# Kernel optimization log

Hardware: AMD Instinct MI355X
Metric: run time of the kernel (lower is better)

The kernel has to match this reference:

```python
import jax, jax.numpy as jnp
import numpy as np

T_STEPS = 128
N_RAYS = 16384
RAY_EXT = 10.0  # ray_ext_factor


def _posenc(x, n_freq=4):
    # x: (...,3) in [-1,1] -> (...,3 + 3*2*n_freq) = (...,27)
    feats = [x]
    for k in range(n_freq):
        f = (2.0 ** k) * jnp.pi
        feats.append(jnp.sin(f * x))
        feats.append(jnp.cos(f * x))
    return jnp.concatenate(feats, -1)


def _sh_deg2(d):
    # real spherical harmonics, degree 0 and 1 (4 coeffs), d unit vectors (...,3)
    x, y, z = d[..., 0], d[..., 1], d[..., 2]
    c0 = 0.28209479177387814
    c1 = 0.4886025119029199
    return jnp.stack([jnp.full_like(x, c0), c1 * y, c1 * z, c1 * x], -1)


def _forward(rays_o, rays_d, tnoise, aabb, W1, b1, W2, b2, Wc1, bc1, Wc2, bc2):
    # --- ray-AABB intersection (slab method), RayBundle.intersect_aabb ---
    inv_d = 1.0 / rays_d
    t0 = (aabb[0] - rays_o) * inv_d
    t1 = (aabb[1] - rays_o) * inv_d
    tnear = jnp.maximum(jnp.max(jnp.minimum(t0, t1), -1, keepdims=True), 0.0)  # (N,1)
    tfar = jnp.min(jnp.maximum(t0, t1), -1, keepdims=True)                      # (N,1)
    active = (tfar > tnear).astype(rays_o.dtype)  # active_mask; masking replaces compaction

    # --- StratifiedRayStepSampler: ts (T,N,1) ---
    T = tnoise.shape[0]
    base = (jnp.arange(T, dtype=rays_o.dtype)[:, None, None] + tnoise) / T
    ts = tnear[None] + (tfar - tnear)[None] * base
    xyz = rays_o[None] + ts * rays_d[None]  # (T,N,3)

    # --- vol.sample(xyz, ynm, return_color=True): density + color MLP ---
    xn = 2.0 * (xyz - aabb[0]) / (aabb[1] - aabb[0]) - 1.0
    enc = _posenc(xn)                             # (T,N,27)
    h = jax.nn.relu(enc @ W1 + b1)                # (T,N,64)
    dh = h @ W2 + b2                              # (T,N,16)
    sigma = jnp.exp(dh[..., :1])                  # (T,N,1) density
    feat = dh[..., 1:]                            # (T,N,15)
    dnorm = jnp.linalg.norm(rays_d, axis=-1, keepdims=True)  # (N,1)
    ynm = _sh_deg2(rays_d / dnorm)                # encode_raydir -> (N,4)
    ynm = jnp.broadcast_to(ynm[None], (T,) + ynm.shape)      # expand to (T,N,4)
    hc = jax.nn.relu(jnp.concatenate([feat, ynm], -1) @ Wc1 + bc1)
    rgb = jax.nn.sigmoid(hc @ Wc2 + bc2)          # (T,N,3)

    # --- integrate_timesteps: transmittance-weighted compositing ---
    tfinal = tfar * RAY_EXT
    delta = jnp.concatenate([ts[1:] - ts[:-1], tfinal[None] - ts[-1:]], 0)  # (T,N,1)
    sd = sigma * delta * dnorm[None]
    alpha = 1.0 - jnp.exp(-sd)
    trans = jnp.exp(-(jnp.cumsum(sd, 0) - sd))    # exclusive cumsum transmittance
    w = trans * alpha * active[None]              # (T,N,1); inactive rays -> zero maps

    color = jnp.sum(w * rgb, 0)                   # color_map  (N,3)
    alpha_map = jnp.sum(w, 0)                     # alpha_map  (N,1)
    return jnp.concatenate([color, alpha_map], -1)  # rgba (N,4)


def setup_inputs() -> dict:
    key = jax.random.key(0)
    ks = jax.random.split(key, 8)
    # origins on a sphere of radius 2.5 around the unit aabb, aimed at points inside it
    o = jax.random.normal(ks[0], (N_RAYS, 3), jnp.float32)
    o = 2.5 * o / jnp.linalg.norm(o, axis=-1, keepdims=True)
    tgt = jax.random.uniform(ks[1], (N_RAYS, 3), jnp.float32, -0.5, 0.5)
    d = tgt - o
    d = d / jnp.linalg.norm(d, axis=-1, keepdims=True)
    aabb = jnp.array([[-1.0, -1.0, -1.0], [1.0, 1.0, 1.0]], jnp.float32)
    tnoise = jax.random.uniform(ks[2], (T_STEPS, N_RAYS, 1), jnp.float32)
    s1, s2, s3, s4 = 27 ** -0.5, 64 ** -0.5, 19 ** -0.5, 64 ** -0.5
    return {
        'rays_o': o, 'rays_d': d, 'tnoise': tnoise, 'aabb': aabb,
        'W1': jax.random.normal(ks[3], (27, 64), jnp.float32) * s1,
        'b1': jnp.zeros((64,), jnp.float32),
        'W2': jax.random.normal(ks[4], (64, 16), jnp.float32) * (0.1 * s2),
        'b2': jnp.zeros((16,), jnp.float32),
        'Wc1': jax.random.normal(ks[5], (19, 64), jnp.float32) * s3,
        'bc1': jnp.zeros((64,), jnp.float32),
        'Wc2': jax.random.normal(ks[6], (64, 3), jnp.float32) * s4,
        'bc2': jnp.zeros((3,), jnp.float32),
    }


def reference(rays_o, rays_d, tnoise, aabb, W1, b1, W2, b2, Wc1, bc1, Wc2, bc2):
    return _forward(rays_o, rays_d, tnoise, aabb, W1, b1, W2, b2, Wc1, bc1, Wc2, bc2)
```

## Files before the change

### kernel.cpp

```cpp
#include <hip/hip_runtime.h>
#include <stdint.h>

#define N_RAYS  16384
#define T_STEPS 128
#define RPW   16
#define WAVES 4
#define TSEG  16

typedef _Float16 half8  __attribute__((ext_vector_type(8)));
typedef _Float16 half4  __attribute__((ext_vector_type(4)));
typedef __fp16   fp16x2 __attribute__((ext_vector_type(2)));
typedef float    float4_ __attribute__((ext_vector_type(4)));

#define H_W2K   2048
#define H_WC1K  3072
#define H_WC2K  4096
#define F32_CV  2560
#define F32_BC2 2880
#define F32_S0  2896
#define F32_PART 4096

__device__ __forceinline__ uint32_t pk(float a, float b) {
    fp16x2 h = __builtin_amdgcn_cvt_pkrtz(a, b);
    return __builtin_bit_cast(uint32_t, h);
}
__device__ __forceinline__ uint32_t pkr(float a, float b) {
    fp16x2 h = __builtin_amdgcn_cvt_pkrtz(a, b);
    fp16x2 z = {(__fp16)0.f, (__fp16)0.f};
    fp16x2 m = __builtin_elementwise_max(h, z);
    return __builtin_bit_cast(uint32_t, m);
}
__device__ __forceinline__ half4 mk4(uint32_t lo, uint32_t hi) {
    union { uint32_t u[2]; half4 h; } v;
    v.u[0] = lo; v.u[1] = hi;
    return v.h;
}

__global__ void prep_weights(const float* __restrict__ W1, const float* __restrict__ b1,
                             const float* __restrict__ W2, const float* __restrict__ b2,
                             const float* __restrict__ Wc1, const float* __restrict__ bc1,
                             const float* __restrict__ Wc2, const float* __restrict__ bc2,
                             void* __restrict__ ws) {
    _Float16* wh = (_Float16*)ws;
    float*    wf = (float*)ws;
    int frag = blockIdx.x;
    int lane = threadIdx.x;
    int mm = lane & 15, q = lane >> 4;
    if (frag < 4) {
        int tau = frag;
        int n = tau * 16 + mm;
        for (int j = 0; j < 8; ++j) {
            float w;
            if (j < 6)      w = W1[(3 + 6 * q + j) * 64 + n];
            else if (j == 6) w = (q == 0) ? W1[0 * 64 + n] : (q == 1) ? W1[2 * 64 + n] : 0.f;
            else             w = (q == 0) ? W1[1 * 64 + n] : (q == 1) ? b1[n] : 0.f;
            wh[(tau * 64 + lane) * 8 + j] = (_Float16)w;
        }
    } else if (frag < 8) {
        int tau = frag - 4;
        for (int j = 0; j < 4; ++j) {
            int k = 16 * tau + 4 * q + j;
            wh[H_W2K + (tau * 64 + lane) * 4 + j] = (_Float16)W2[k * 16 + mm];
        }
    } else if (frag < 12) {
        int tau = frag - 8;
        int n2 = tau * 16 + mm;
        for (int j = 0; j < 4; ++j) {
            int k = 4 * q + j;
            float w = (k == 0) ? 0.f : Wc1[(k - 1) * 64 + n2];
            wh[H_WC1K + (tau * 64 + lane) * 4 + j] = (_Float16)w;
        }
    } else if (frag < 16) {
        int tau = frag - 12;
        for (int j = 0; j < 4; ++j) {
            int k = 16 * tau + 4 * q + j;
            wh[H_WC2K + (tau * 64 + lane) * 4 + j] =
                (_Float16)((mm < 3) ? Wc2[k * 3 + mm] : 0.f);
        }
    } else {
        int n = lane;
        wf[F32_CV + 0 * 64 + n] = Wc1[15 * 64 + n];
        wf[F32_CV + 1 * 64 + n] = Wc1[16 * 64 + n];
        wf[F32_CV + 2 * 64 + n] = Wc1[17 * 64 + n];
        wf[F32_CV + 3 * 64 + n] = Wc1[18 * 64 + n];
        float cc = bc1[n];
        for (int c = 0; c < 15; ++c) cc += b2[1 + c] * Wc1[c * 64 + n];
        wf[F32_CV + 4 * 64 + n] = cc;
        if (lane < 16) wf[F32_BC2 + lane] = (lane < 3) ? bc2[lane] : 0.f;
        if (lane == 0) wf[F32_S0] = b2[0];
    }
}

__global__ __launch_bounds__(256, 4)
void render_kernel(const float* __restrict__ rays_o, const float* __restrict__ rays_d,
                   const float* __restrict__ tnoise, const float* __restrict__ aabb,
                   void* __restrict__ ws, float* __restrict__ out) {
    __shared__ float sComb[WAVES][RPW][5];

    const int tid  = threadIdx.x;
    const int wv   = tid >> 6;
    const int lane = tid & 63;
    const int m    = lane & 15;
    const int q    = lane >> 4;
    const int half_ = blockIdx.x & 1;
    const int rb   = blockIdx.x >> 1;
    const int r    = rb * RPW + m;

    const half8* wsv   = (const half8*)ws;
    const half4* w2k   = (const half4*)((const _Float16*)ws + H_W2K);
    const half4* wc1k  = (const half4*)((const _Float16*)ws + H_WC1K);
    const half4* wc2k  = (const half4*)((const _Float16*)ws + H_WC2K);
    const float* wsf   = (const float*)ws;
    half8 fW1[4];
    half4 fW2[4], fWc1[4], fWc2[4];
    #pragma unroll
    for (int i = 0; i < 4; ++i) fW1[i]  = wsv[i * 64 + lane];
    #pragma unroll
    for (int i = 0; i < 4; ++i) fW2[i]  = w2k[i * 64 + lane];
    #pragma unroll
    for (int i = 0; i < 4; ++i) fWc1[i] = wc1k[i * 64 + lane];
    #pragma unroll
    for (int i = 0; i < 4; ++i) fWc2[i] = wc2k[i * 64 + lane];
    const float4_ binit = ((const float4_*)(wsf + F32_BC2))[q];
    const float s0b = wsf[F32_S0];

    float o0 = rays_o[r * 3 + 0], o1 = rays_o[r * 3 + 1], o2 = rays_o[r * 3 + 2];
    float d0 = rays_d[r * 3 + 0], d1 = rays_d[r * 3 + 1], d2 = rays_d[r * 3 + 2];
    float a00 = aabb[0], a01 = aabb[1], a02 = aabb[2];
    float a10 = aabb[3], a11 = aabb[4], a12 = aabb[5];

    float i0 = 1.0f / d0, i1 = 1.0f / d1, i2 = 1.0f / d2;
    float u0 = (a00 - o0) * i0, v0 = (a10 - o0) * i0;
    float u1 = (a01 - o1) * i1, v1 = (a11 - o1) * i1;
    float u2 = (a02 - o2) * i2, v2 = (a02 * 0.0f + a12 - o2) * i2;
    float tnear = fmaxf(fmaxf(fmaxf(fminf(u0, v0), fminf(u1, v1)), fminf(u2, v2)), 0.0f);
    float tfar  = fminf(fminf(fmaxf(u0, v0), fmaxf(u1, v1)), fmaxf(u2, v2));
    bool active = (tfar > tnear);
    float dt = tfar - tnear;
    float dt128 = dt * (1.0f / 128.0f);

    float dn  = sqrtf(d0 * d0 + d1 * d1 + d2 * d2);
    float idn = 1.0f / dn;
    const float c0sh = 0.28209479177387814f;
    const float c1sh = 0.4886025119029199f;
    float y1 = c1sh * d1 * idn, y2 = c1sh * d2 * idn, y3 = c1sh * d0 * idn;

    float4_ cv[4];
    #pragma unroll
    for (int tau = 0; tau < 4; ++tau) {
        #pragma unroll
        for (int reg = 0; reg < 4; ++reg) {
            int n = tau * 16 + 4 * q + reg;
            float c = wsf[F32_CV + 4 * 64 + n];
            c = fmaf(c0sh, wsf[F32_CV + 0 * 64 + n], c);
            c = fmaf(y1,   wsf[F32_CV + 1 * 64 + n], c);
            c = fmaf(y2,   wsf[F32_CV + 2 * 64 + n], c);
            c = fmaf(y3,   wsf[F32_CV + 3 * 64 + n], c);
            cv[tau][reg] = c;
        }
    }

    float qs = 0.5f * (float)(1 << q);
    float sc0 = 2.0f / (a10 - a00), of0 = -a00 * sc0 - 1.0f;
    float sc1 = 2.0f / (a11 - a01), of1 = -a01 * sc1 - 1.0f;
    float sc2 = 2.0f / (a12 - a02), of2 = -a02 * sc2 - 1.0f;
    float scq0 = sc0 * qs, ofq0 = of0 * qs;
    float scq1 = sc1 * qs, ofq1 = of1 * qs;
    float scq2 = sc2 * qs, ofq2 = of2 * qs;

    const float4_ z4 = {0.f, 0.f, 0.f, 0.f};
    const bool q0 = (q == 0), q1 = (q == 1);

    float trans = 1.0f, sdtot = 0.0f, wacc = 0.0f;
    float cacc0 = 0.0f, cacc1 = 0.0f, cacc2 = 0.0f;

    const int tbase = half_ * 64 + wv * TSEG;
    float nA = tnoise[(tbase + 0) * N_RAYS + r];
    float nB = tnoise[(tbase + 1) * N_RAYS + r];

    #pragma unroll 1
    for (int tt = 0; tt < TSEG; tt += 2) {
        const int t0 = tbase + tt, t1 = t0 + 1;
        float nC = (t0 + 2 < T_STEPS) ? tnoise[(t0 + 2) * N_RAYS + r] : 0.0f;
        float nD = (t0 + 3 < T_STEPS) ? tnoise[(t0 + 3) * N_RAYS + r] : 0.0f;
        float ts0 = fmaf((float)t0 + nA, dt128, tnear);
        float ts1 = fmaf((float)t1 + nB, dt128, tnear);
        float ts2 = fmaf((float)(t0 + 2) + nC, dt128, tnear);
        float tsP[2] = {ts0, ts1};
        float deltaP[2];
        deltaP[0] = ts1 - ts0;
        deltaP[1] = (t1 < T_STEPS - 1) ? (ts2 - ts1) : fmaf(tfar, 10.0f, -ts1);
        nA = nC; nB = nD;

        float dhx[2];
        float4_ rgbP[2];

        #pragma unroll
        for (int p = 0; p < 2; ++p) {
            float x = fmaf(tsP[p], d0, o0);
            float y = fmaf(tsP[p], d1, o1);
            float z = fmaf(tsP[p], d2, o2);
            float xr0 = fmaf(x, scq0, ofq0);
            float xr1 = fmaf(y, scq1, ofq1);
            float xr2 = fmaf(z, scq2, ofq2);
            float s0 = __builtin_amdgcn_sinf(xr0);
            float s1 = __builtin_amdgcn_sinf(xr1);
            float s2 = __builtin_amdgcn_sinf(xr2);
            float cA = __builtin_amdgcn_cosf(xr0);
            float cB = __builtin_amdgcn_cosf(xr1);
            float cC = __builtin_amdgcn_cosf(xr2);
            float e6 = q0 ? (xr0 + xr0) : (q1 ? xr2 : 0.0f);
            float e7 = q0 ? (xr1 + xr1) : (q1 ? 1.0f : 0.0f);
            union { uint32_t u[4]; half8 h; } xf_;
            xf_.u[0] = pk(s0, s1); xf_.u[1] = pk(s2, cA);
            xf_.u[2] = pk(cB, cC); xf_.u[3] = pk(e6, e7);
            half8 xf = xf_.h;

            float4_ h0 = __builtin_amdgcn_mfma_f32_16x16x32_f16(fW1[0], xf, z4, 0, 0, 0);
            float4_ h1 = __builtin_amdgcn_mfma_f32_16x16x32_f16(fW1[1], xf, z4, 0, 0, 0);
            float4_ h2 = __builtin_amdgcn_mfma_f32_16x16x32_f16(fW1[2], xf, z4, 0, 0, 0);
            float4_ h3 = __builtin_amdgcn_mfma_f32_16x16x32_f16(fW1[3], xf, z4, 0, 0, 0);

            half4 hB0 = mk4(pkr(h0.x, h0.y), pkr(h0.z, h0.w));
            half4 hB1 = mk4(pkr(h1.x, h1.y), pkr(h1.z, h1.w));
            half4 hB2 = mk4(pkr(h2.x, h2.y), pkr(h2.z, h2.w));
            half4 hB3 = mk4(pkr(h3.x, h3.y), pkr(h3.z, h3.w));

            float4_ dh = __builtin_amdgcn_mfma_f32_16x16x16f16(fW2[0], hB0, z4, 0, 0, 0);
            dh = __builtin_amdgcn_mfma_f32_16x16x16f16(fW2[1], hB1, dh, 0, 0, 0);
            dh = __builtin_amdgcn_mfma_f32_16x16x16f16(fW2[2], hB2, dh, 0, 0, 0);
            dh = __builtin_amdgcn_mfma_f32_16x16x16f16(fW2[3], hB3, dh, 0, 0, 0);
            dhx[p] = dh.x;

            half4 fb = mk4(pk(dh.x, dh.y), pk(dh.z, dh.w));

            float4_ t0v = __builtin_amdgcn_mfma_f32_16x16x16f16(fWc1[0], fb, cv[0], 0, 0, 0);
            float4_ t1v = __builtin_amdgcn_mfma_f32_16x16x16f16(fWc1[1], fb, cv[1], 0, 0, 0);
            float4_ t2v = __builtin_amdgcn_mfma_f32_16x16x16f16(fWc1[2], fb, cv[2], 0, 0, 0);
            float4_ t3v = __builtin_amdgcn_mfma_f32_16x16x16f16(fWc1[3], fb, cv[3], 0, 0, 0);

            half4 cB0 = mk4(pkr(t0v.x, t0v.y), pkr(t0v.z, t0v.w));
            half4 cB1 = mk4(pkr(t1v.x, t1v.y), pkr(t1v.z, t1v.w));
            half4 cB2 = mk4(pkr(t2v.x, t2v.y), pkr(t2v.z, t2v.w));
            half4 cB3 = mk4(pkr(t3v.x, t3v.y), pkr(t3v.z, t3v.w));

            float4_ rgb = __builtin_amdgcn_mfma_f32_16x16x16f16(fWc2[0], cB0, binit, 0, 0, 0);
            rgb = __builtin_amdgcn_mfma_f32_16x16x16f16(fWc2[1], cB1, rgb, 0, 0, 0);
            rgb = __builtin_amdgcn_mfma_f32_16x16x16f16(fWc2[2], cB2, rgb, 0, 0, 0);
            rgb = __builtin_amdgcn_mfma_f32_16x16x16f16(fWc2[3], cB3, rgb, 0, 0, 0);
            rgbP[p] = rgb;
        }

        if (q == 0) {
            #pragma unroll
            for (int p = 0; p < 2; ++p) {
                float sigma = __expf(dhx[p] + s0b);
                float sd = sigma * deltaP[p] * dn;
                float e = __expf(-sd);
                float alpha = 1.0f - e;
                float w = trans * alpha;
                float rr = __builtin_amdgcn_rcpf(1.0f + __expf(-rgbP[p].x));
                float rg = __builtin_amdgcn_rcpf(1.0f + __expf(-rgbP[p].y));
                float rb = __builtin_amdgcn_rcpf(1.0f + __expf(-rgbP[p].z));
                cacc0 = fmaf(w, rr, cacc0);
                cacc1 = fmaf(w, rg, cacc1);
                cacc2 = fmaf(w, rb, cacc2);
                wacc += w;
                trans *= e;
                sdtot += sd;
            }
        }
    }

    if (q == 0) {
        sComb[wv][m][0] = sdtot;
        sComb[wv][m][1] = wacc;
        sComb[wv][m][2] = cacc0;
        sComb[wv][m][3] = cacc1;
        sComb[wv][m][4] = cacc2;
    }
    __syncthreads();

    if (tid < RPW) {
        float P = 1.0f, C0 = 0.0f, C1 = 0.0f, C2 = 0.0f, WS = 0.0f, SD = 0.0f;
        #pragma unroll
        for (int s = 0; s < WAVES; ++s) {
            C0 = fmaf(P, sComb[s][tid][2], C0);
            C1 = fmaf(P, sComb[s][tid][3], C1);
            C2 = fmaf(P, sComb[s][tid][4], C2);
            WS = fmaf(P, sComb[s][tid][1], WS);
            SD += sComb[s][tid][0];
            P *= __expf(-sComb[s][tid][0]);
        }
        const int rg = rb * RPW + tid;
        float* part = (float*)ws + F32_PART + (half_ * N_RAYS + rg) * 6;
        part[0] = SD;
        part[1] = WS;
        part[2] = C0;
        part[3] = C1;
        part[4] = C2;
        part[5] = active ? 1.0f : 0.0f;
    }
}

__global__ __launch_bounds__(256)
void combine_kernel(const void* __restrict__ ws, float* __restrict__ out) {
    int r = blockIdx.x * 256 + threadIdx.x;
    const float* pa = (const float*)ws + F32_PART + r * 6;
    const float* pb = (const float*)ws + F32_PART + (N_RAYS + r) * 6;
    float P = __expf(-pa[0]);
    float act = pa[5];
    out[r * 4 + 0] = fmaf(P, pb[2], pa[2]) * act;
    out[r * 4 + 1] = fmaf(P, pb[3], pa[3]) * act;
    out[r * 4 + 2] = fmaf(P, pb[4], pa[4]) * act;
    out[r * 4 + 3] = fmaf(P, pb[1], pa[1]) * act;
}

extern "C" void kernel_launch(void* const* d_in, const int* in_sizes, int n_in,
                              void* d_out, int out_size, void* d_ws, size_t ws_size,
                              hipStream_t stream) {
    const float* rays_o = (const float*)d_in[0];
    const float* rays_d = (const float*)d_in[1];
    const float* tnoise = (const float*)d_in[2];
    const float* aabb   = (const float*)d_in[3];
    const float* W1  = (const float*)d_in[4];
    const float* b1  = (const float*)d_in[5];
    const float* W2  = (const float*)d_in[6];
    const float* b2  = (const float*)d_in[7];
    const float* Wc1 = (const float*)d_in[8];
    const float* bc1 = (const float*)d_in[9];
    const float* Wc2 = (const float*)d_in[10];
    const float* bc2 = (const float*)d_in[11];

    prep_weights<<<dim3(17), dim3(64), 0, stream>>>(W1, b1, W2, b2, Wc1, bc1, Wc2, bc2, d_ws);

    dim3 grid(2 * N_RAYS / RPW);
    dim3 block(WAVES * 64);
    render_kernel<<<grid, block, 0, stream>>>(rays_o, rays_d, tnoise, aabb, d_ws,
                                              (float*)d_out);

    combine_kernel<<<dim3(N_RAYS / 256), dim3(256), 0, stream>>>(d_ws, (float*)d_out);
}
```

Baseline: 124.8 us.

## Drop weight-prep kernel, load weights inline and split MFMA accumulation chains

Removes the separate prep_weights launch. Each render wave now gathers and converts the MLP weights to fp16 fragments directly from the raw inputs, and folds the b2/Wc1 constant vector in place. This removes one kernel launch and its serialization before the render kernel. In exchange, every block does many more scattered scalar global loads and conversions at startup, and the bias-fold fma loop is recomputed per thread. Separately, the 4-deep dependent MFMA chains for the second and output layers are split into two independent chains that are summed, to shorten the dependency latency.

```diff
diff --git a/kernel.cpp b/kernel.cpp
--- a/kernel.cpp
+++ b/kernel.cpp
@@ -12,13 +12,7 @@
 typedef __fp16   fp16x2 __attribute__((ext_vector_type(2)));
 typedef float    float4_ __attribute__((ext_vector_type(4)));
 
-#define H_W2K   2048
-#define H_WC1K  3072
-#define H_WC2K  4096
-#define F32_CV  2560
-#define F32_BC2 2880
-#define F32_S0  2896
-#define F32_PART 4096
+#define F32_PART 0
 
 __device__ __forceinline__ uint32_t pk(float a, float b) {
     fp16x2 h = __builtin_amdgcn_cvt_pkrtz(a, b);
@@ -36,65 +30,14 @@
     return v.h;
 }
 
-__global__ void prep_weights(const float* __restrict__ W1, const float* __restrict__ b1,
-                             const float* __restrict__ W2, const float* __restrict__ b2,
-                             const float* __restrict__ Wc1, const float* __restrict__ bc1,
-                             const float* __restrict__ Wc2, const float* __restrict__ bc2,
-                             void* __restrict__ ws) {
-    _Float16* wh = (_Float16*)ws;
-    float*    wf = (float*)ws;
-    int frag = blockIdx.x;
-    int lane = threadIdx.x;
-    int mm = lane & 15, q = lane >> 4;
-    if (frag < 4) {
-        int tau = frag;
-        int n = tau * 16 + mm;
-        for (int j = 0; j < 8; ++j) {
-            float w;
-            if (j < 6)      w = W1[(3 + 6 * q + j) * 64 + n];
-            else if (j == 6) w = (q == 0) ? W1[0 * 64 + n] : (q == 1) ? W1[2 * 64 + n] : 0.f;
-            else             w = (q == 0) ? W1[1 * 64 + n] : (q == 1) ? b1[n] : 0.f;
-            wh[(tau * 64 + lane) * 8 + j] = (_Float16)w;
-        }
-    } else if (frag < 8) {
-        int tau = frag - 4;
-        for (int j = 0; j < 4; ++j) {
-            int k = 16 * tau + 4 * q + j;
-            wh[H_W2K + (tau * 64 + lane) * 4 + j] = (_Float16)W2[k * 16 + mm];
-        }
-    } else if (frag < 12) {
-        int tau = frag - 8;
-        int n2 = tau * 16 + mm;
-        for (int j = 0; j < 4; ++j) {
-            int k = 4 * q + j;
-            float w = (k == 0) ? 0.f : Wc1[(k - 1) * 64 + n2];
-            wh[H_WC1K + (tau * 64 + lane) * 4 + j] = (_Float16)w;
-        }
-    } else if (frag < 16) {
-        int tau = frag - 12;
-        for (int j = 0; j < 4; ++j) {
-            int k = 16 * tau + 4 * q + j;
-            wh[H_WC2K + (tau * 64 + lane) * 4 + j] =
-                (_Float16)((mm < 3) ? Wc2[k * 3 + mm] : 0.f);
-        }
-    } else {
-        int n = lane;
-        wf[F32_CV + 0 * 64 + n] = Wc1[15 * 64 + n];
-        wf[F32_CV + 1 * 64 + n] = Wc1[16 * 64 + n];
-        wf[F32_CV + 2 * 64 + n] = Wc1[17 * 64 + n];
-        wf[F32_CV + 3 * 64 + n] = Wc1[18 * 64 + n];
-        float cc = bc1[n];
-        for (int c = 0; c < 15; ++c) cc += b2[1 + c] * Wc1[c * 64 + n];
-        wf[F32_CV + 4 * 64 + n] = cc;
-        if (lane < 16) wf[F32_BC2 + lane] = (lane < 3) ? bc2[lane] : 0.f;
-        if (lane == 0) wf[F32_S0] = b2[0];
-    }
-}
-
 __global__ __launch_bounds__(256, 4)
 void render_kernel(const float* __restrict__ rays_o, const float* __restrict__ rays_d,
                    const float* __restrict__ tnoise, const float* __restrict__ aabb,
-                   void* __restrict__ ws, float* __restrict__ out) {
+                   const float* __restrict__ W1, const float* __restrict__ b1,
+                   const float* __restrict__ W2, const float* __restrict__ b2,
+                   const float* __restrict__ Wc1, const float* __restrict__ bc1,
+                   const float* __restrict__ Wc2, const float* __restrict__ bc2,
+                   float* __restrict__ wsp, float* __restrict__ out) {
     __shared__ float sComb[WAVES][RPW][5];
 
     const int tid  = threadIdx.x;
@@ -105,24 +48,7 @@
     const int half_ = blockIdx.x & 1;
     const int rb   = blockIdx.x >> 1;
     const int r    = rb * RPW + m;
-
-    const half8* wsv   = (const half8*)ws;
-    const half4* w2k   = (const half4*)((const _Float16*)ws + H_W2K);
-    const half4* wc1k  = (const half4*)((const _Float16*)ws + H_WC1K);
-    const half4* wc2k  = (const half4*)((const _Float16*)ws + H_WC2K);
-    const float* wsf   = (const float*)ws;
-    half8 fW1[4];
-    half4 fW2[4], fWc1[4], fWc2[4];
-    #pragma unroll
-    for (int i = 0; i < 4; ++i) fW1[i]  = wsv[i * 64 + lane];
-    #pragma unroll
-    for (int i = 0; i < 4; ++i) fW2[i]  = w2k[i * 64 + lane];
-    #pragma unroll
-    for (int i = 0; i < 4; ++i) fWc1[i] = wc1k[i * 64 + lane];
-    #pragma unroll
-    for (int i = 0; i < 4; ++i) fWc2[i] = wc2k[i * 64 + lane];
-    const float4_ binit = ((const float4_*)(wsf + F32_BC2))[q];
-    const float s0b = wsf[F32_S0];
+    const bool q0 = (q == 0), q1 = (q == 1);
 
     float o0 = rays_o[r * 3 + 0], o1 = rays_o[r * 3 + 1], o2 = rays_o[r * 3 + 2];
     float d0 = rays_d[r * 3 + 0], d1 = rays_d[r * 3 + 1], d2 = rays_d[r * 3 + 2];
@@ -132,7 +58,7 @@
     float i0 = 1.0f / d0, i1 = 1.0f / d1, i2 = 1.0f / d2;
     float u0 = (a00 - o0) * i0, v0 = (a10 - o0) * i0;
     float u1 = (a01 - o1) * i1, v1 = (a11 - o1) * i1;
-    float u2 = (a02 - o2) * i2, v2 = (a02 * 0.0f + a12 - o2) * i2;
+    float u2 = (a02 - o2) * i2, v2 = (a12 - o2) * i2;
     float tnear = fmaxf(fmaxf(fmaxf(fminf(u0, v0), fminf(u1, v1)), fminf(u2, v2)), 0.0f);
     float tfar  = fminf(fminf(fmaxf(u0, v0), fmaxf(u1, v1)), fmaxf(u2, v2));
     bool active = (tfar > tnear);
@@ -145,20 +71,66 @@
     const float c1sh = 0.4886025119029199f;
     float y1 = c1sh * d1 * idn, y2 = c1sh * d2 * idn, y3 = c1sh * d0 * idn;
 
+    half8 fW1[4];
+    #pragma unroll
+    for (int tau = 0; tau < 4; ++tau) {
+        int n = tau * 16 + m;
+        half8 hh;
+        #pragma unroll
+        for (int j = 0; j < 6; ++j) hh[j] = (_Float16)W1[(3 + 6 * q + j) * 64 + n];
+        hh[6] = (_Float16)(q0 ? W1[0 * 64 + n] : (q1 ? W1[2 * 64 + n] : 0.f));
+        hh[7] = (_Float16)(q0 ? W1[1 * 64 + n] : (q1 ? b1[n] : 0.f));
+        fW1[tau] = hh;
+    }
+    half4 fW2[4], fWc1[4], fWc2[4];
+    #pragma unroll
+    for (int tau = 0; tau < 4; ++tau) {
+        half4 hh;
+        #pragma unroll
+        for (int j = 0; j < 4; ++j)
+            hh[j] = (_Float16)W2[(16 * tau + 4 * q + j) * 16 + m];
+        fW2[tau] = hh;
+        int n2 = tau * 16 + m;
+        half4 hc;
+        #pragma unroll
+        for (int j = 0; j < 4; ++j) {
+            int k = 4 * q + j;
+            hc[j] = (_Float16)((k == 0) ? 0.f : Wc1[(k - 1) * 64 + n2]);
+        }
+        fWc1[tau] = hc;
+        half4 h2;
+        #pragma unroll
+        for (int j = 0; j < 4; ++j) {
+            int k = 16 * tau + 4 * q + j;
+            h2[j] = (_Float16)((m < 3) ? Wc2[k * 3 + m] : 0.f);
+        }
+        fWc2[tau] = h2;
+    }
+
     float4_ cv[4];
     #pragma unroll
     for (int tau = 0; tau < 4; ++tau) {
         #pragma unroll
         for (int reg = 0; reg < 4; ++reg) {
             int n = tau * 16 + 4 * q + reg;
-            float c = wsf[F32_CV + 4 * 64 + n];
-            c = fmaf(c0sh, wsf[F32_CV + 0 * 64 + n], c);
-            c = fmaf(y1,   wsf[F32_CV + 1 * 64 + n], c);
-            c = fmaf(y2,   wsf[F32_CV + 2 * 64 + n], c);
-            c = fmaf(y3,   wsf[F32_CV + 3 * 64 + n], c);
+            float c = bc1[n];
+            #pragma unroll
+            for (int cc = 0; cc < 15; ++cc)
+                c = fmaf(b2[1 + cc], Wc1[cc * 64 + n], c);
+            c = fmaf(c0sh, Wc1[15 * 64 + n], c);
+            c = fmaf(y1,   Wc1[16 * 64 + n], c);
+            c = fmaf(y2,   Wc1[17 * 64 + n], c);
+            c = fmaf(y3,   Wc1[18 * 64 + n], c);
             cv[tau][reg] = c;
         }
     }
+    float4_ binit;
+    #pragma unroll
+    for (int reg = 0; reg < 4; ++reg) {
+        int idx = 4 * q + reg;
+        binit[reg] = (idx < 3) ? bc2[idx] : 0.f;
+    }
+    const float s0b = b2[0];
 
     float qs = 0.5f * (float)(1 << q);
     float sc0 = 2.0f / (a10 - a00), of0 = -a00 * sc0 - 1.0f;
@@ -169,7 +141,6 @@
     float scq2 = sc2 * qs, ofq2 = of2 * qs;
 
     const float4_ z4 = {0.f, 0.f, 0.f, 0.f};
-    const bool q0 = (q == 0), q1 = (q == 1);
 
     float trans = 1.0f, sdtot = 0.0f, wacc = 0.0f;
     float cacc0 = 0.0f, cacc1 = 0.0f, cacc2 = 0.0f;
@@ -226,10 +197,11 @@
             half4 hB2 = mk4(pkr(h2.x, h2.y), pkr(h2.z, h2.w));
             half4 hB3 = mk4(pkr(h3.x, h3.y), pkr(h3.z, h3.w));
 
-            float4_ dh = __builtin_amdgcn_mfma_f32_16x16x16f16(fW2[0], hB0, z4, 0, 0, 0);
-            dh = __builtin_amdgcn_mfma_f32_16x16x16f16(fW2[1], hB1, dh, 0, 0, 0);
-            dh = __builtin_amdgcn_mfma_f32_16x16x16f16(fW2[2], hB2, dh, 0, 0, 0);
-            dh = __builtin_amdgcn_mfma_f32_16x16x16f16(fW2[3], hB3, dh, 0, 0, 0);
+            float4_ dA = __builtin_amdgcn_mfma_f32_16x16x16f16(fW2[0], hB0, z4, 0, 0, 0);
+            float4_ dB = __builtin_amdgcn_mfma_f32_16x16x16f16(fW2[1], hB1, z4, 0, 0, 0);
+            dA = __builtin_amdgcn_mfma_f32_16x16x16f16(fW2[2], hB2, dA, 0, 0, 0);
+            dB = __builtin_amdgcn_mfma_f32_16x16x16f16(fW2[3], hB3, dB, 0, 0, 0);
+            float4_ dh = dA + dB;
             dhx[p] = dh.x;
 
             half4 fb = mk4(pk(dh.x, dh.y), pk(dh.z, dh.w));
@@ -244,11 +216,11 @@
             half4 cB2 = mk4(pkr(t2v.x, t2v.y), pkr(t2v.z, t2v.w));
             half4 cB3 = mk4(pkr(t3v.x, t3v.y), pkr(t3v.z, t3v.w));
 
-            float4_ rgb = __builtin_amdgcn_mfma_f32_16x16x16f16(fWc2[0], cB0, binit, 0, 0, 0);
-            rgb = __builtin_amdgcn_mfma_f32_16x16x16f16(fWc2[1], cB1, rgb, 0, 0, 0);
-            rgb = __builtin_amdgcn_mfma_f32_16x16x16f16(fWc2[2], cB2, rgb, 0, 0, 0);
-            rgb = __builtin_amdgcn_mfma_f32_16x16x16f16(fWc2[3], cB3, rgb, 0, 0, 0);
-            rgbP[p] = rgb;
+            float4_ rA = __builtin_amdgcn_mfma_f32_16x16x16f16(fWc2[0], cB0, binit, 0, 0, 0);
+            float4_ rB = __builtin_amdgcn_mfma_f32_16x16x16f16(fWc2[1], cB1, z4, 0, 0, 0);
+            rA = __builtin_amdgcn_mfma_f32_16x16x16f16(fWc2[2], cB2, rA, 0, 0, 0);
+            rB = __builtin_amdgcn_mfma_f32_16x16x16f16(fWc2[3], cB3, rB, 0, 0, 0);
+            rgbP[p] = rA + rB;
         }
 
         if (q == 0) {
@@ -293,7 +265,7 @@
             P *= __expf(-sComb[s][tid][0]);
         }
         const int rg = rb * RPW + tid;
-        float* part = (float*)ws + F32_PART + (half_ * N_RAYS + rg) * 6;
+        float* part = wsp + F32_PART + (half_ * N_RAYS + rg) * 6;
         part[0] = SD;
         part[1] = WS;
         part[2] = C0;
@@ -304,10 +276,10 @@
 }
 
 __global__ __launch_bounds__(256)
-void combine_kernel(const void* __restrict__ ws, float* __restrict__ out) {
+void combine_kernel(const float* __restrict__ wsp, float* __restrict__ out) {
     int r = blockIdx.x * 256 + threadIdx.x;
-    const float* pa = (const float*)ws + F32_PART + r * 6;
-    const float* pb = (const float*)ws + F32_PART + (N_RAYS + r) * 6;
+    const float* pa = wsp + F32_PART + r * 6;
+    const float* pb = wsp + F32_PART + (N_RAYS + r) * 6;
     float P = __expf(-pa[0]);
     float act = pa[5];
     out[r * 4 + 0] = fmaf(P, pb[2], pa[2]) * act;
@@ -332,12 +304,12 @@
     const float* Wc2 = (const float*)d_in[10];
     const float* bc2 = (const float*)d_in[11];
 
-    prep_weights<<<dim3(17), dim3(64), 0, stream>>>(W1, b1, W2, b2, Wc1, bc1, Wc2, bc2, d_ws);
-
     dim3 grid(2 * N_RAYS / RPW);
     dim3 block(WAVES * 64);
-    render_kernel<<<grid, block, 0, stream>>>(rays_o, rays_d, tnoise, aabb, d_ws,
-                                              (float*)d_out);
-
-    combine_kernel<<<dim3(N_RAYS / 256), dim3(256), 0, stream>>>(d_ws, (float*)d_out);
-}
+    render_kernel<<<grid, block, 0, stream>>>(rays_o, rays_d, tnoise, aabb,
+                                              W1, b1, W2, b2, Wc1, bc1, Wc2, bc2,
+                                              (float*)d_ws, (float*)d_out);
+
+    combine_kernel<<<dim3(N_RAYS / 256), dim3(256), 0, stream>>>((const float*)d_ws,
+                                                                 (float*)d_out);
+}
```

After: 419.5 us. 236% more time.
